# Kernel tuning notes

Hardware: AMD Instinct MI355X
Metric: run time of the kernel (lower is better)

The kernel has to match this reference:

```python
import jax, jax.numpy as jnp
import numpy as np

B, S, D = 4, 128, 4096
H, KV, HD = 32, 8, 128
REP = H // KV  # GQA repeat factor = 4


def setup_inputs() -> dict:
    key = jax.random.key(0)
    ks = jax.random.split(key, 10)
    scale = 0.02
    x = jax.random.normal(ks[0], (B, S, D), dtype=jnp.float32)
    # projection weights stored as (in, out) so y = x @ W + b (== torch Linear)
    wq = jax.random.normal(ks[1], (D, H * HD), dtype=jnp.float32) * scale
    bq = jax.random.normal(ks[2], (H * HD,), dtype=jnp.float32) * scale
    wk = jax.random.normal(ks[3], (D, KV * HD), dtype=jnp.float32) * scale
    bk = jax.random.normal(ks[4], (KV * HD,), dtype=jnp.float32) * scale
    wv = jax.random.normal(ks[5], (D, KV * HD), dtype=jnp.float32) * scale
    bv = jax.random.normal(ks[6], (KV * HD,), dtype=jnp.float32) * scale
    wo = jax.random.normal(ks[7], (H * HD, D), dtype=jnp.float32) * scale
    bo = jax.random.normal(ks[8], (D,), dtype=jnp.float32) * scale
    # rotary frequencies: theta=10000, half-dim = HD//2 = 64
    inv_freq = 1.0 / (10000.0 ** (jnp.arange(0, HD, 2, dtype=jnp.float32) / HD))
    t = jnp.arange(S, dtype=jnp.float32)
    angles = jnp.outer(t, inv_freq)  # (S, 64)
    freqs_cos = jnp.cos(angles)
    freqs_sin = jnp.sin(angles)
    # additive causal mask (S, S): 0 on/below diagonal, -inf above
    mask = jnp.where(jnp.tril(jnp.ones((S, S), dtype=bool)), 0.0, -jnp.inf).astype(jnp.float32)
    cache_k = jnp.zeros((B, S, KV, HD), dtype=jnp.float32)
    cache_v = jnp.zeros((B, S, KV, HD), dtype=jnp.float32)
    return {
        "x": x, "start_pos": 0, "freqs_cos": freqs_cos, "freqs_sin": freqs_sin,
        "mask": mask, "cache_k": cache_k, "cache_v": cache_v,
        "wq": wq, "bq": bq, "wk": wk, "bk": bk, "wv": wv, "bv": bv,
        "wo": wo, "bo": bo,
    }


def _rope(t, cos, sin):
    # t: (B, S, h, HD); treat last dim as HD//2 complex pairs (real, imag)
    tr = t.reshape(*t.shape[:-1], HD // 2, 2)
    tre, tim = tr[..., 0], tr[..., 1]
    c = cos[None, :, None, :]  # (1, S, 1, HD//2)
    s = sin[None, :, None, :]
    out_re = tre * c - tim * s
    out_im = tre * s + tim * c
    return jnp.stack([out_re, out_im], axis=-1).reshape(t.shape)


def reference(x, start_pos, freqs_cos, freqs_sin, mask, cache_k, cache_v,
              wq, bq, wk, bk, wv, bv, wo, bo):
    bsz, seq_len, _ = x.shape
    q = (x @ wq + bq).reshape(bsz, seq_len, H, HD)
    k = (x @ wk + bk).reshape(bsz, seq_len, KV, HD)
    v = (x @ wv + bv).reshape(bsz, seq_len, KV, HD)
    q = _rope(q, freqs_cos, freqs_sin)
    k = _rope(k, freqs_cos, freqs_sin)
    # KV-cache append (functional)
    cache_k = cache_k.at[:bsz, start_pos:start_pos + seq_len].set(k)
    cache_v = cache_v.at[:bsz, start_pos:start_pos + seq_len].set(v)
    keys = cache_k[:bsz, :start_pos + seq_len]    # (B, T, KV, HD)
    vals = cache_v[:bsz, :start_pos + seq_len]
    # GQA head expansion (repeat_interleave on head dim)
    keys = jnp.repeat(keys, REP, axis=2)          # (B, T, H, HD)
    vals = jnp.repeat(vals, REP, axis=2)
    scale = 1.0 / jnp.sqrt(jnp.float32(HD))
    scores = jnp.einsum('bqhd,bkhd->bhqk', q, keys) * scale + mask
    attn = jax.nn.softmax(scores, axis=-1)
    out = jnp.einsum('bhqk,bkhd->bqhd', attn, vals).reshape(bsz, seq_len, H * HD)
    return out @ wo + bo
```

## Files before the change

### kernel.cpp

```cpp
#include <hip/hip_runtime.h>
#include <math.h>


#define B_   4
#define S_   128
#define D_   4096
#define H_   32
#define KV_  8
#define HD_  128
#define M_   (B_ * S_)
#define NQKV 6144
#define SCALE_ 0.088388347648318447f

typedef _Float16 half_t;
typedef half_t f16x8 __attribute__((ext_vector_type(8)));
typedef float  f32x4 __attribute__((ext_vector_type(4)));

__device__ inline void load_lds16(const void* g, void* l) {
    __builtin_amdgcn_global_load_lds((const __attribute__((address_space(1))) void*)g,
                                     (__attribute__((address_space(3))) void*)l,
                                     16, 0, 0);
}

__device__ void transpose_tile(const float* __restrict__ src, int Nsrc, int nsrc0,
                               int ndst0, int k0, int Ntot,
                               half_t* __restrict__ Wt, void* ldsraw) {
    float (*tile)[132] = (float(*)[132])ldsraw;
    const int t = threadIdx.x;
#pragma unroll
    for (int p = 0; p < 8; ++p) {
        int idx = t + p * 256;
        int r = idx >> 5, c4 = idx & 31;
        *(float4*)&tile[r][c4 * 4] =
            *(const float4*)&src[(size_t)(k0 + r) * Nsrc + nsrc0 + c4 * 4];
    }
    __syncthreads();
    const int n = t >> 1, kh = t & 1;
    __align__(16) half_t hs[32];
#pragma unroll
    for (int i = 0; i < 32; ++i)
        hs[i] = (half_t)tile[kh * 32 + i][n];
    size_t ob = ((size_t)(k0 >> 6) * Ntot + ndst0 + n) * 64 + kh * 32;
#pragma unroll
    for (int u = 0; u < 4; ++u)
        *(uint4*)&Wt[ob + u * 8] = *(uint4*)&hs[u * 8];
}

__device__ void gemm_tile(const half_t* __restrict__ A16, const half_t* __restrict__ Wt,
                          float* __restrict__ Part, int N, int m0, int n0,
                          int zi, int kslice, char* lds) {
    half_t (*As)[64] = (half_t(*)[64])lds;
    half_t (*Bs)[64] = (half_t(*)[64])(lds + 16384);
    const int tid = threadIdx.x;
    const int kbase = zi * kslice;
    const int lane = tid & 63;
    const int quad = lane >> 4, l16 = lane & 15;
    const int w = tid >> 6;
    const int wm = (w & 1) * 64, wn = (w >> 1) * 64;
    const int tB = tid & 192;

    f32x4 acc[4][4] = {};

    for (int kc = kbase; kc < kbase + kslice; kc += 64) {
        const half_t* Bslab = Wt + ((size_t)(kc >> 6) * N + n0) * 64;
#pragma unroll
        for (int p = 0; p < 4; ++p) {
            int tb = p * 256 + tB;
            int task = tb + lane;
            int r = task >> 3;
            int os = (task ^ r) & 7;
            load_lds16(&A16[(size_t)(m0 + r) * 4096 + kc + os * 8], (half_t*)As + tb * 8);
            load_lds16(&Bslab[(size_t)r * 64 + os * 8],             (half_t*)Bs + tb * 8);
        }
        __syncthreads();
#pragma unroll
        for (int kk = 0; kk < 2; ++kk) {
            f16x8 af[4], bf[4];
#pragma unroll
            for (int i = 0; i < 4; ++i) {
                int ra = wm + i * 16 + l16;
                int rb = wn + i * 16 + l16;
                int L = kk * 4 + quad;
                af[i] = *(const f16x8*)&As[ra][(L ^ (ra & 7)) * 8];
                bf[i] = *(const f16x8*)&Bs[rb][(L ^ (rb & 7)) * 8];
            }
#pragma unroll
            for (int i = 0; i < 4; ++i)
#pragma unroll
                for (int j = 0; j < 4; ++j)
                    acc[i][j] = __builtin_amdgcn_mfma_f32_16x16x32_f16(af[i], bf[j], acc[i][j], 0, 0, 0);
        }
        __syncthreads();
    }
    float* Cp = Part + (size_t)zi * ((size_t)M_ * N);
#pragma unroll
    for (int i = 0; i < 4; ++i)
#pragma unroll
        for (int j = 0; j < 4; ++j) {
            int col = n0 + wn + j * 16 + l16;
            int rowb = m0 + wm + i * 16 + quad * 4;
#pragma unroll
            for (int rg = 0; rg < 4; ++rg)
                Cp[(size_t)(rowb + rg) * N + col] = acc[i][j][rg];
        }
}

__global__ __launch_bounds__(256)
void prep_qkv(const float* __restrict__ wq, const float* __restrict__ wk,
              const float* __restrict__ wv, const float* __restrict__ x,
              half_t* __restrict__ Wt, half_t* __restrict__ x16) {
    __shared__ __align__(16) char lds[33792];
    const int bx = blockIdx.x;
    if (bx < 3072) {
        int nt = bx % 48, kt = bx / 48;
        const float* src; int Nsrc, ns0, nd0;
        if (nt < 32)      { src = wq; Nsrc = 4096; ns0 = nt * 128;        nd0 = nt * 128; }
        else if (nt < 40) { src = wk; Nsrc = 1024; ns0 = (nt - 32) * 128; nd0 = 4096 + (nt - 32) * 128; }
        else              { src = wv; Nsrc = 1024; ns0 = (nt - 40) * 128; nd0 = 5120 + (nt - 40) * 128; }
        transpose_tile(src, Nsrc, ns0, nd0, kt * 64, NQKV, Wt, lds);
    } else {
        int i0 = (bx - 3072) * 1024 + threadIdx.x;
#pragma unroll
        for (int j = 0; j < 4; ++j) {
            int i = i0 + j * 256;
            float4 f = ((const float4*)x)[i];
            __align__(8) half_t h4[4] = {(half_t)f.x, (half_t)f.y, (half_t)f.z, (half_t)f.w};
            ((uint2*)x16)[i] = *(uint2*)h4;
        }
    }
}

__global__ __launch_bounds__(256, 3)
void gemm_qkv_pack(const half_t* __restrict__ x16, const half_t* __restrict__ Wt,
                   float* __restrict__ Part, int kslice, int gemmBlocks,
                   const float* __restrict__ wo, half_t* __restrict__ WtO) {
    __shared__ __align__(16) char lds[33792];
    const int bx = blockIdx.x;
    if (bx < gemmBlocks) {
        int nb = bx % 48, mb = (bx / 48) & 3, zi = bx / 192;
        gemm_tile(x16, Wt, Part, NQKV, mb * 128, nb * 128, zi, kslice, lds);
    } else {
        int t = bx - gemmBlocks;
        int nt = t & 31, kt = t >> 5;
        transpose_tile(wo, 4096, nt * 128, nt * 128, kt * 64, 4096, WtO, lds);
    }
}

__global__ __launch_bounds__(256)
void wo_trans(const float* __restrict__ wo, half_t* __restrict__ WtO) {
    __shared__ __align__(16) char lds[33792];
    int nt = blockIdx.x & 31, kt = blockIdx.x >> 5;
    transpose_tile(wo, 4096, nt * 128, nt * 128, kt * 64, 4096, WtO, lds);
}

__global__ __launch_bounds__(256, 3)
void gemm_o(const half_t* __restrict__ a16, const half_t* __restrict__ WtO,
            float* __restrict__ Part, int kslice) {
    __shared__ __align__(16) char lds[33792];
    gemm_tile(a16, WtO, Part, 4096, blockIdx.y * 128, blockIdx.x * 128,
              blockIdx.z, kslice, lds);
}

__global__ void qkv_reduce_rope(const float* __restrict__ Part, int nz,
                                const float* __restrict__ bq, const float* __restrict__ bk,
                                const float* __restrict__ bv,
                                const float* __restrict__ fc, const float* __restrict__ fs,
                                half_t* __restrict__ q16, half_t* __restrict__ k16,
                                half_t* __restrict__ vt16) {
    const int row = blockIdx.y;
    const int col = (blockIdx.x * 256 + threadIdx.x) * 2;
    const size_t off = (size_t)row * NQKV + col;
    float2 s = *(const float2*)&Part[off];
    for (int z = 1; z < nz; ++z) {
        float2 p = *(const float2*)&Part[(size_t)z * (M_ * NQKV) + off];
        s.x += p.x; s.y += p.y;
    }
    float2 bi;
    if (col < 4096)      bi = *(const float2*)&bq[col];
    else if (col < 5120) bi = *(const float2*)&bk[col - 4096];
    else                 bi = *(const float2*)&bv[col - 5120];
    s.x += bi.x; s.y += bi.y;
    if (col < 5120) {
        int d2 = (col >> 1) & 63;
        int i = row & 127;
        float c = fc[i * 64 + d2], sn = fs[i * 64 + d2];
        float re = s.x, im = s.y;
        s.x = re * c - im * sn;
        s.y = re * sn + im * c;
    }
    __align__(4) half_t hh[2] = {(half_t)s.x, (half_t)s.y};
    if (col < 4096) {
        *(unsigned int*)&q16[(size_t)row * 4096 + col] = *(unsigned int*)hh;
    } else if (col < 5120) {
        *(unsigned int*)&k16[(size_t)row * 1024 + (col - 4096)] = *(unsigned int*)hh;
    } else {
        int c = col - 5120;
        int kv = c >> 7, d = c & 127;
        int b = row >> 7, i = row & 127;
        size_t base = ((size_t)(b * 8 + kv) * 128 + d) * 128 + i;
        vt16[base]       = hh[0];
        vt16[base + 128] = hh[1];
    }
}

__global__ __launch_bounds__(256, 2)
void fused_attn(const half_t* __restrict__ q16, const half_t* __restrict__ k16,
                const half_t* __restrict__ vt16, half_t* __restrict__ a16) {
    __shared__ __align__(16) half_t Qs[32][136];
    __shared__ __align__(16) half_t Ks[128][136];
    __shared__ float Ps[32][132];
    __shared__ float red[32][16];

    const int tid = threadIdx.x;
    const int qi = blockIdx.x & 3, h = (blockIdx.x >> 2) & 31, b = blockIdx.x >> 7;
    const int kv = h >> 2;
    const int qbase = qi * 32;
    const int lane = tid & 63, w = tid >> 6;
    const int quad = lane >> 4, l16 = lane & 15;
    const int m0 = (w & 1) * 16, half64 = (w >> 1) * 64;

#pragma unroll
    for (int p = 0; p < 2; ++p) {
        int task = tid + p * 256;
        int r = task >> 4, c = task & 15;
        *(uint4*)&Qs[r][c * 8] =
            *(const uint4*)&q16[((size_t)(b * 128 + qbase + r) * 32 + h) * 128 + c * 8];
    }
#pragma unroll
    for (int p = 0; p < 8; ++p) {
        int task = tid + p * 256;
        int r = task >> 4, c = task & 15;
        *(uint4*)&Ks[r][c * 8] =
            *(const uint4*)&k16[((size_t)(b * 128 + r) * 8 + kv) * 128 + c * 8];
    }
    __syncthreads();

    f32x4 s[4] = {};
#pragma unroll
    for (int kc = 0; kc < 4; ++kc) {
        f16x8 af = *(const f16x8*)&Qs[m0 + l16][kc * 32 + quad * 8];
#pragma unroll
        for (int jb = 0; jb < 4; ++jb) {
            f16x8 bf = *(const f16x8*)&Ks[half64 + jb * 16 + l16][kc * 32 + quad * 8];
            s[jb] = __builtin_amdgcn_mfma_f32_16x16x32_f16(af, bf, s[jb], 0, 0, 0);
        }
    }
#pragma unroll
    for (int jb = 0; jb < 4; ++jb) {
        int j = half64 + jb * 16 + l16;
#pragma unroll
        for (int rg = 0; rg < 4; ++rg) {
            int row = m0 + quad * 4 + rg;
            Ps[row][j] = (j <= qbase + row) ? s[jb][rg] * SCALE_ : -1e30f;
        }
    }
    __syncthreads();

    const int r = tid >> 3, seg = tid & 7;
    float mx = -1e30f;
#pragma unroll
    for (int i = 0; i < 16; ++i) mx = fmaxf(mx, Ps[r][seg * 16 + i]);
    red[r][seg] = mx;
    __syncthreads();

    uint4 vstage[8];
#pragma unroll
    for (int p = 0; p < 8; ++p) {
        int task = tid + p * 256;
        int rr = task >> 4, c = task & 15;
        vstage[p] = *(const uint4*)&vt16[((size_t)(b * 8 + kv) * 128 + rr) * 128 + c * 8];
    }
    float m = red[r][0];
#pragma unroll
    for (int i = 1; i < 8; ++i) m = fmaxf(m, red[r][i]);
    float sum = 0.f;
#pragma unroll
    for (int i = 0; i < 16; ++i) {
        float e = __expf(Ps[r][seg * 16 + i] - m);
        Ps[r][seg * 16 + i] = e;
        sum += e;
    }
    red[r][8 + seg] = sum;
#pragma unroll
    for (int p = 0; p < 8; ++p) {
        int task = tid + p * 256;
        int rr = task >> 4, c = task & 15;
        *(uint4*)&Ks[rr][c * 8] = vstage[p];
    }
    __syncthreads();

    float tot = 0.f;
#pragma unroll
    for (int i = 0; i < 8; ++i) tot += red[r][8 + i];
    float inv = 1.0f / tot;
#pragma unroll
    for (int i = 0; i < 16; ++i)
        Qs[r][seg * 16 + i] = (half_t)(Ps[r][seg * 16 + i] * inv);
    __syncthreads();

    f32x4 o[4] = {};
#pragma unroll
    for (int jc = 0; jc < 4; ++jc) {
        f16x8 af = *(const f16x8*)&Qs[m0 + l16][jc * 32 + quad * 8];
#pragma unroll
        for (int db = 0; db < 4; ++db) {
            f16x8 bf = *(const f16x8*)&Ks[half64 + db * 16 + l16][jc * 32 + quad * 8];
            o[db] = __builtin_amdgcn_mfma_f32_16x16x32_f16(af, bf, o[db], 0, 0, 0);
        }
    }
#pragma unroll
    for (int db = 0; db < 4; ++db) {
        int d = half64 + db * 16 + l16;
#pragma unroll
        for (int rg = 0; rg < 4; ++rg) {
            int row = m0 + quad * 4 + rg;
            a16[(size_t)(b * 128 + qbase + row) * 4096 + h * 128 + d] = (half_t)o[db][rg];
        }
    }
}

__global__ void o_reduce(const float* __restrict__ Part, int nz,
                         const float* __restrict__ bo, float* __restrict__ out) {
    const size_t off = (size_t)(blockIdx.x * 256 + threadIdx.x) * 4;
    float4 s = *(const float4*)&Part[off];
    for (int z = 1; z < nz; ++z) {
        float4 p = *(const float4*)&Part[(size_t)z * (M_ * 4096) + off];
        s.x += p.x; s.y += p.y; s.z += p.z; s.w += p.w;
    }
    float4 b = *(const float4*)&bo[off & 4095];
    s.x += b.x; s.y += b.y; s.z += b.z; s.w += b.w;
    *(float4*)&out[off] = s;
}

extern "C" void kernel_launch(void* const* d_in, const int* in_sizes, int n_in,
                              void* d_out, int out_size, void* d_ws, size_t ws_size,
                              hipStream_t stream) {
    const float* x    = (const float*)d_in[0];
    const float* fc   = (const float*)d_in[2];
    const float* fs   = (const float*)d_in[3];
    const float* wq   = (const float*)d_in[7];
    const float* bq   = (const float*)d_in[8];
    const float* wk   = (const float*)d_in[9];
    const float* bk   = (const float*)d_in[10];
    const float* wv   = (const float*)d_in[11];
    const float* bv   = (const float*)d_in[12];
    const float* wo   = (const float*)d_in[13];
    const float* bo   = (const float*)d_in[14];
    float* out = (float*)d_out;

    half_t* x16  = (half_t*)d_ws;
    half_t* a16  = x16 + 2097152;
    half_t* q16  = a16 + 2097152;
    half_t* k16  = q16 + 2097152;
    half_t* vt16 = k16 + 524288;
    half_t* Wt   = vt16 + 524288;

    const size_t fixedB = 65011712;
    const size_t fixedA = fixedB + (size_t)16777216 * 2;
    int z; bool packed;
    if      (ws_size >= fixedA + 4 * (size_t)12582912) { packed = true;  z = 4; }
    else if (ws_size >= fixedA + 2 * (size_t)12582912) { packed = true;  z = 2; }
    else if (ws_size >= fixedB + 4 * (size_t)12582912) { packed = false; z = 4; }
    else                                               { packed = false; z = 2; }
    half_t* WtO  = packed ? Wt + 25165824 : Wt;
    float*  Part = (float*)((char*)d_ws + (packed ? fixedA : fixedB));
    const int kslice = 4096 / z;

    prep_qkv<<<3584, 256, 0, stream>>>(wq, wk, wv, x, Wt, x16);

    gemm_qkv_pack<<<192 * z + (packed ? 2048 : 0), 256, 0, stream>>>(
        x16, Wt, Part, kslice, 192 * z, wo, WtO);

    qkv_reduce_rope<<<dim3(12, 512), 256, 0, stream>>>(Part, z, bq, bk, bv, fc, fs,
                                                       q16, k16, vt16);
    if (!packed)
        wo_trans<<<2048, 256, 0, stream>>>(wo, WtO);

    fused_attn<<<512, 256, 0, stream>>>(q16, k16, vt16, a16);

    gemm_o<<<dim3(32, 4, z), 256, 0, stream>>>(a16, WtO, Part, kslice);
    o_reduce<<<2048, 256, 0, stream>>>(Part, z, bo, out);
}
```

Measured before the change: 295.3 us.

## Fuse split-K reductions, bias and RoPE into GEMM epilogues; overlap Wo transpose with attention

```diff
diff --git a/kernel.cpp b/kernel.cpp
--- a/kernel.cpp
+++ b/kernel.cpp
@@ -44,65 +44,6 @@
 #pragma unroll
     for (int u = 0; u < 4; ++u)
         *(uint4*)&Wt[ob + u * 8] = *(uint4*)&hs[u * 8];
-}
-
-__device__ void gemm_tile(const half_t* __restrict__ A16, const half_t* __restrict__ Wt,
-                          float* __restrict__ Part, int N, int m0, int n0,
-                          int zi, int kslice, char* lds) {
-    half_t (*As)[64] = (half_t(*)[64])lds;
-    half_t (*Bs)[64] = (half_t(*)[64])(lds + 16384);
-    const int tid = threadIdx.x;
-    const int kbase = zi * kslice;
-    const int lane = tid & 63;
-    const int quad = lane >> 4, l16 = lane & 15;
-    const int w = tid >> 6;
-    const int wm = (w & 1) * 64, wn = (w >> 1) * 64;
-    const int tB = tid & 192;
-
-    f32x4 acc[4][4] = {};
-
-    for (int kc = kbase; kc < kbase + kslice; kc += 64) {
-        const half_t* Bslab = Wt + ((size_t)(kc >> 6) * N + n0) * 64;
-#pragma unroll
-        for (int p = 0; p < 4; ++p) {
-            int tb = p * 256 + tB;
-            int task = tb + lane;
-            int r = task >> 3;
-            int os = (task ^ r) & 7;
-            load_lds16(&A16[(size_t)(m0 + r) * 4096 + kc + os * 8], (half_t*)As + tb * 8);
-            load_lds16(&Bslab[(size_t)r * 64 + os * 8],             (half_t*)Bs + tb * 8);
-        }
-        __syncthreads();
-#pragma unroll
-        for (int kk = 0; kk < 2; ++kk) {
-            f16x8 af[4], bf[4];
-#pragma unroll
-            for (int i = 0; i < 4; ++i) {
-                int ra = wm + i * 16 + l16;
-                int rb = wn + i * 16 + l16;
-                int L = kk * 4 + quad;
-                af[i] = *(const f16x8*)&As[ra][(L ^ (ra & 7)) * 8];
-                bf[i] = *(const f16x8*)&Bs[rb][(L ^ (rb & 7)) * 8];
-            }
-#pragma unroll
-            for (int i = 0; i < 4; ++i)
-#pragma unroll
-                for (int j = 0; j < 4; ++j)
-                    acc[i][j] = __builtin_amdgcn_mfma_f32_16x16x32_f16(af[i], bf[j], acc[i][j], 0, 0, 0);
-        }
-        __syncthreads();
-    }
-    float* Cp = Part + (size_t)zi * ((size_t)M_ * N);
-#pragma unroll
-    for (int i = 0; i < 4; ++i)
-#pragma unroll
-        for (int j = 0; j < 4; ++j) {
-            int col = n0 + wn + j * 16 + l16;
-            int rowb = m0 + wm + i * 16 + quad * 4;
-#pragma unroll
-            for (int rg = 0; rg < 4; ++rg)
-                Cp[(size_t)(rowb + rg) * N + col] = acc[i][j][rg];
-        }
 }
 
 __global__ __launch_bounds__(256)
@@ -130,86 +71,156 @@
     }
 }
 
-__global__ __launch_bounds__(256, 3)
-void gemm_qkv_pack(const half_t* __restrict__ x16, const half_t* __restrict__ Wt,
-                   float* __restrict__ Part, int kslice, int gemmBlocks,
-                   const float* __restrict__ wo, half_t* __restrict__ WtO) {
-    __shared__ __align__(16) char lds[33792];
-    const int bx = blockIdx.x;
-    if (bx < gemmBlocks) {
-        int nb = bx % 48, mb = (bx / 48) & 3, zi = bx / 192;
-        gemm_tile(x16, Wt, Part, NQKV, mb * 128, nb * 128, zi, kslice, lds);
+__global__ __launch_bounds__(512)
+void gemm_qkv_fused(const half_t* __restrict__ x16, const half_t* __restrict__ Wt,
+                    const float* __restrict__ bq, const float* __restrict__ bk,
+                    const float* __restrict__ bv, const float* __restrict__ fc,
+                    const float* __restrict__ fs, half_t* __restrict__ q16,
+                    half_t* __restrict__ k16, half_t* __restrict__ vt16) {
+    __shared__ __align__(16) char lds[67584];
+    const int tid = threadIdx.x;
+    const int nb = blockIdx.x % 48, mb = blockIdx.x / 48;
+    const int m0 = mb * 128, n0 = nb * 128;
+    const int g = tid >> 8;
+    const int lane = tid & 63;
+    const int quad = lane >> 4, l16 = lane & 15;
+    const int w4 = (tid >> 6) & 3;
+    const int wm = (w4 & 1) * 64, wn = (w4 >> 1) * 64;
+    const int tB = tid & 192;
+
+    half_t (*As)[64] = (half_t(*)[64])(lds + g * 32768);
+    half_t (*Bs)[64] = (half_t(*)[64])(lds + g * 32768 + 16384);
+
+    f32x4 acc[4][4] = {};
+    const int kend = g * 2048 + 2048;
+    for (int kc = g * 2048; kc < kend; kc += 64) {
+        const half_t* Bslab = Wt + ((size_t)(kc >> 6) * NQKV + n0) * 64;
+#pragma unroll
+        for (int p = 0; p < 4; ++p) {
+            int tb = p * 256 + tB;
+            int task = tb + lane;
+            int r = task >> 3;
+            int os = (task ^ r) & 7;
+            load_lds16(&x16[(size_t)(m0 + r) * 4096 + kc + os * 8], (half_t*)As + tb * 8);
+            load_lds16(&Bslab[(size_t)r * 64 + os * 8],             (half_t*)Bs + tb * 8);
+        }
+        __syncthreads();
+#pragma unroll
+        for (int kk = 0; kk < 2; ++kk) {
+            f16x8 af[4], bf[4];
+#pragma unroll
+            for (int i = 0; i < 4; ++i) {
+                int ra = wm + i * 16 + l16;
+                int rb = wn + i * 16 + l16;
+                int L = kk * 4 + quad;
+                af[i] = *(const f16x8*)&As[ra][(L ^ (ra & 7)) * 8];
+                bf[i] = *(const f16x8*)&Bs[rb][(L ^ (rb & 7)) * 8];
+            }
+#pragma unroll
+            for (int i = 0; i < 4; ++i)
+#pragma unroll
+                for (int j = 0; j < 4; ++j)
+                    acc[i][j] = __builtin_amdgcn_mfma_f32_16x16x32_f16(af[i], bf[j], acc[i][j], 0, 0, 0);
+        }
+        __syncthreads();
+    }
+
+    float (*Tf)[132] = (float(*)[132])lds;
+    if (g == 1) {
+#pragma unroll
+        for (int i = 0; i < 4; ++i)
+#pragma unroll
+            for (int j = 0; j < 4; ++j)
+#pragma unroll
+                for (int rg = 0; rg < 4; ++rg)
+                    Tf[wm + i * 16 + quad * 4 + rg][wn + j * 16 + l16] = acc[i][j][rg];
+    }
+    __syncthreads();
+    if (g == 0) {
+#pragma unroll
+        for (int i = 0; i < 4; ++i)
+#pragma unroll
+            for (int j = 0; j < 4; ++j)
+#pragma unroll
+                for (int rg = 0; rg < 4; ++rg)
+                    acc[i][j][rg] += Tf[wm + i * 16 + quad * 4 + rg][wn + j * 16 + l16];
+    }
+
+    if (n0 < 5120) {
+        if (g == 0) {
+            const bool isQ = n0 < 4096;
+            const float* bias = isQ ? bq : bk;
+            const int bOff = isQ ? 0 : 4096;
+            half_t* dst = isQ ? q16 : k16;
+            const int ldd = isQ ? 4096 : 1024;
+#pragma unroll
+            for (int i = 0; i < 4; ++i)
+#pragma unroll
+                for (int j = 0; j < 4; ++j) {
+                    const int col = n0 + wn + j * 16 + l16;
+                    const int d2 = (col >> 1) & 63;
+                    const float bcol = bias[col - bOff];
+#pragma unroll
+                    for (int rg = 0; rg < 4; ++rg) {
+                        const int row = m0 + wm + i * 16 + quad * 4 + rg;
+                        float v = acc[i][j][rg] + bcol;
+                        float o = __shfl_xor(v, 1);
+                        const int iloc = row & 127;
+                        const float c = fc[iloc * 64 + d2], sn = fs[iloc * 64 + d2];
+                        float ov = (l16 & 1) ? (o * sn + v * c)
+                                             : (v * c - o * sn);
+                        float o2 = __shfl_xor(ov, 1);
+                        if (!(l16 & 1)) {
+                            __align__(4) half_t hh[2] = {(half_t)ov, (half_t)o2};
+                            *(unsigned int*)&dst[(size_t)row * ldd + (col - bOff)] =
+                                *(unsigned int*)hh;
+                        }
+                    }
+                }
+        }
     } else {
-        int t = bx - gemmBlocks;
-        int nt = t & 31, kt = t >> 5;
-        transpose_tile(wo, 4096, nt * 128, nt * 128, kt * 64, 4096, WtO, lds);
-    }
-}
-
-__global__ __launch_bounds__(256)
-void wo_trans(const float* __restrict__ wo, half_t* __restrict__ WtO) {
-    __shared__ __align__(16) char lds[33792];
-    int nt = blockIdx.x & 31, kt = blockIdx.x >> 5;
-    transpose_tile(wo, 4096, nt * 128, nt * 128, kt * 64, 4096, WtO, lds);
-}
-
-__global__ __launch_bounds__(256, 3)
-void gemm_o(const half_t* __restrict__ a16, const half_t* __restrict__ WtO,
-            float* __restrict__ Part, int kslice) {
-    __shared__ __align__(16) char lds[33792];
-    gemm_tile(a16, WtO, Part, 4096, blockIdx.y * 128, blockIdx.x * 128,
-              blockIdx.z, kslice, lds);
-}
-
-__global__ void qkv_reduce_rope(const float* __restrict__ Part, int nz,
-                                const float* __restrict__ bq, const float* __restrict__ bk,
-                                const float* __restrict__ bv,
-                                const float* __restrict__ fc, const float* __restrict__ fs,
-                                half_t* __restrict__ q16, half_t* __restrict__ k16,
-                                half_t* __restrict__ vt16) {
-    const int row = blockIdx.y;
-    const int col = (blockIdx.x * 256 + threadIdx.x) * 2;
-    const size_t off = (size_t)row * NQKV + col;
-    float2 s = *(const float2*)&Part[off];
-    for (int z = 1; z < nz; ++z) {
-        float2 p = *(const float2*)&Part[(size_t)z * (M_ * NQKV) + off];
-        s.x += p.x; s.y += p.y;
-    }
-    float2 bi;
-    if (col < 4096)      bi = *(const float2*)&bq[col];
-    else if (col < 5120) bi = *(const float2*)&bk[col - 4096];
-    else                 bi = *(const float2*)&bv[col - 5120];
-    s.x += bi.x; s.y += bi.y;
-    if (col < 5120) {
-        int d2 = (col >> 1) & 63;
-        int i = row & 127;
-        float c = fc[i * 64 + d2], sn = fs[i * 64 + d2];
-        float re = s.x, im = s.y;
-        s.x = re * c - im * sn;
-        s.y = re * sn + im * c;
-    }
-    __align__(4) half_t hh[2] = {(half_t)s.x, (half_t)s.y};
-    if (col < 4096) {
-        *(unsigned int*)&q16[(size_t)row * 4096 + col] = *(unsigned int*)hh;
-    } else if (col < 5120) {
-        *(unsigned int*)&k16[(size_t)row * 1024 + (col - 4096)] = *(unsigned int*)hh;
-    } else {
-        int c = col - 5120;
-        int kv = c >> 7, d = c & 127;
-        int b = row >> 7, i = row & 127;
-        size_t base = ((size_t)(b * 8 + kv) * 128 + d) * 128 + i;
-        vt16[base]       = hh[0];
-        vt16[base + 128] = hh[1];
+        __syncthreads();
+        half_t (*Th)[136] = (half_t(*)[136])lds;
+        if (g == 0) {
+#pragma unroll
+            for (int i = 0; i < 4; ++i)
+#pragma unroll
+                for (int j = 0; j < 4; ++j) {
+                    const int cl = wn + j * 16 + l16;
+                    const float bcol = bv[n0 - 5120 + cl];
+#pragma unroll
+                    for (int rg = 0; rg < 4; ++rg)
+                        Th[wm + i * 16 + quad * 4 + rg][cl] = (half_t)(acc[i][j][rg] + bcol);
+                }
+        }
+        __syncthreads();
+        const int d = tid >> 2, iq = tid & 3;
+        const int kv = (n0 - 5120) >> 7;
+        __align__(16) half_t hs[32];
+#pragma unroll
+        for (int u = 0; u < 32; ++u) hs[u] = Th[iq * 32 + u][d];
+        size_t base = ((size_t)(mb * 8 + kv) * 128 + d) * 128 + iq * 32;
+#pragma unroll
+        for (int u = 0; u < 4; ++u)
+            *(uint4*)&vt16[base + u * 8] = *(uint4*)&hs[u * 8];
     }
 }
 
 __global__ __launch_bounds__(256, 2)
-void fused_attn(const half_t* __restrict__ q16, const half_t* __restrict__ k16,
-                const half_t* __restrict__ vt16, half_t* __restrict__ a16) {
-    __shared__ __align__(16) half_t Qs[32][136];
-    __shared__ __align__(16) half_t Ks[128][136];
-    __shared__ float Ps[32][132];
-    __shared__ float red[32][16];
+void attn_wo(const half_t* __restrict__ q16, const half_t* __restrict__ k16,
+             const half_t* __restrict__ vt16, half_t* __restrict__ a16,
+             const float* __restrict__ wo, half_t* __restrict__ WtO) {
+    __shared__ __align__(16) char lds[62464];
+    if (blockIdx.x >= 512) {
+        int t = blockIdx.x - 512;
+        transpose_tile(wo, 4096, (t & 31) * 128, (t & 31) * 128, (t >> 5) * 64,
+                       4096, WtO, lds);
+        return;
+    }
+    half_t (*Qs)[136] = (half_t(*)[136])lds;
+    half_t (*Ks)[136] = (half_t(*)[136])(lds + 8704);
+    float (*Ps)[132]  = (float(*)[132])(lds + 43520);
+    float (*red)[16]  = (float(*)[16])(lds + 60416);
 
     const int tid = threadIdx.x;
     const int qi = blockIdx.x & 3, h = (blockIdx.x >> 2) & 31, b = blockIdx.x >> 7;
@@ -319,17 +330,86 @@
     }
 }
 
-__global__ void o_reduce(const float* __restrict__ Part, int nz,
-                         const float* __restrict__ bo, float* __restrict__ out) {
-    const size_t off = (size_t)(blockIdx.x * 256 + threadIdx.x) * 4;
-    float4 s = *(const float4*)&Part[off];
-    for (int z = 1; z < nz; ++z) {
-        float4 p = *(const float4*)&Part[(size_t)z * (M_ * 4096) + off];
-        s.x += p.x; s.y += p.y; s.z += p.z; s.w += p.w;
-    }
-    float4 b = *(const float4*)&bo[off & 4095];
-    s.x += b.x; s.y += b.y; s.z += b.z; s.w += b.w;
-    *(float4*)&out[off] = s;
+__global__ __launch_bounds__(512)
+void gemm_o_fused(const half_t* __restrict__ a16, const half_t* __restrict__ WtO,
+                  const float* __restrict__ bo, float* __restrict__ out) {
+    __shared__ __align__(16) char lds[49152];
+    const int tid = threadIdx.x;
+    const int nb = blockIdx.x & 31, mb = blockIdx.x >> 5;
+    const int m0 = mb * 64, n0 = nb * 128;
+    const int g = tid >> 8;
+    const int lane = tid & 63;
+    const int quad = lane >> 4, l16 = lane & 15;
+    const int w4 = (tid >> 6) & 3;
+    const int wn = w4 * 32;
+    const int tB = tid & 192;
+
+    half_t (*As)[64] = (half_t(*)[64])(lds + g * 24576);
+    half_t (*Bs)[64] = (half_t(*)[64])(lds + g * 24576 + 8192);
+
+    f32x4 acc[4][2] = {};
+    const int kend = g * 2048 + 2048;
+    for (int kc = g * 2048; kc < kend; kc += 64) {
+        const half_t* Bslab = WtO + ((size_t)(kc >> 6) * 4096 + n0) * 64;
+#pragma unroll
+        for (int p = 0; p < 4; ++p) {
+            int tb = p * 256 + tB;
+            int task = tb + lane;
+            int r = task >> 3;
+            int os = (task ^ r) & 7;
+            load_lds16(&Bslab[(size_t)r * 64 + os * 8], (half_t*)Bs + tb * 8);
+            if (p < 2)
+                load_lds16(&a16[(size_t)(m0 + r) * 4096 + kc + os * 8], (half_t*)As + tb * 8);
+        }
+        __syncthreads();
+#pragma unroll
+        for (int kk = 0; kk < 2; ++kk) {
+            f16x8 af[4], bf[2];
+#pragma unroll
+            for (int i = 0; i < 4; ++i) {
+                int ra = i * 16 + l16;
+                af[i] = *(const f16x8*)&As[ra][((kk * 4 + quad) ^ (ra & 7)) * 8];
+            }
+#pragma unroll
+            for (int j = 0; j < 2; ++j) {
+                int rb = wn + j * 16 + l16;
+                bf[j] = *(const f16x8*)&Bs[rb][((kk * 4 + quad) ^ (rb & 7)) * 8];
+            }
+#pragma unroll
+            for (int i = 0; i < 4; ++i)
+#pragma unroll
+                for (int j = 0; j < 2; ++j)
+                    acc[i][j] = __builtin_amdgcn_mfma_f32_16x16x32_f16(af[i], bf[j], acc[i][j], 0, 0, 0);
+        }
+        __syncthreads();
+    }
+
+    float (*Tf)[132] = (float(*)[132])lds;
+    if (g == 1) {
+#pragma unroll
+        for (int i = 0; i < 4; ++i)
+#pragma unroll
+            for (int j = 0; j < 2; ++j)
+#pragma unroll
+                for (int rg = 0; rg < 4; ++rg)
+                    Tf[i * 16 + quad * 4 + rg][wn + j * 16 + l16] = acc[i][j][rg];
+    }
+    __syncthreads();
+    if (g == 0) {
+#pragma unroll
+        for (int i = 0; i < 4; ++i)
+#pragma unroll
+            for (int j = 0; j < 2; ++j) {
+                const int col = n0 + wn + j * 16 + l16;
+                const float bcol = bo[col];
+#pragma unroll
+                for (int rg = 0; rg < 4; ++rg) {
+                    const int row = m0 + i * 16 + quad * 4 + rg;
+                    out[(size_t)row * 4096 + col] =
+                        acc[i][j][rg] + Tf[i * 16 + quad * 4 + rg][wn + j * 16 + l16] + bcol;
+                }
+            }
+    }
 }
 
 extern "C" void kernel_launch(void* const* d_in, const int* in_sizes, int n_in,
@@ -354,30 +434,14 @@
     half_t* k16  = q16 + 2097152;
     half_t* vt16 = k16 + 524288;
     half_t* Wt   = vt16 + 524288;
-
-    const size_t fixedB = 65011712;
-    const size_t fixedA = fixedB + (size_t)16777216 * 2;
-    int z; bool packed;
-    if      (ws_size >= fixedA + 4 * (size_t)12582912) { packed = true;  z = 4; }
-    else if (ws_size >= fixedA + 2 * (size_t)12582912) { packed = true;  z = 2; }
-    else if (ws_size >= fixedB + 4 * (size_t)12582912) { packed = false; z = 4; }
-    else                                               { packed = false; z = 2; }
-    half_t* WtO  = packed ? Wt + 25165824 : Wt;
-    float*  Part = (float*)((char*)d_ws + (packed ? fixedA : fixedB));
-    const int kslice = 4096 / z;
+    half_t* WtO  = Wt;
 
     prep_qkv<<<3584, 256, 0, stream>>>(wq, wk, wv, x, Wt, x16);
 
-    gemm_qkv_pack<<<192 * z + (packed ? 2048 : 0), 256, 0, stream>>>(
-        x16, Wt, Part, kslice, 192 * z, wo, WtO);
-
-    qkv_reduce_rope<<<dim3(12, 512), 256, 0, stream>>>(Part, z, bq, bk, bv, fc, fs,
-                                                       q16, k16, vt16);
-    if (!packed)
-        wo_trans<<<2048, 256, 0, stream>>>(wo, WtO);
-
-    fused_attn<<<512, 256, 0, stream>>>(q16, k16, vt16, a16);
-
-    gemm_o<<<dim3(32, 4, z), 256, 0, stream>>>(a16, WtO, Part, kslice);
-    o_reduce<<<2048, 256, 0, stream>>>(Part, z, bo, out);
-}
+    gemm_qkv_fused<<<192, 512, 0, stream>>>(x16, Wt, bq, bk, bv, fc, fs,
+                                            q16, k16, vt16);
+
+    attn_wo<<<2560, 256, 0, stream>>>(q16, k16, vt16, a16, wo, WtO);
+
+    gemm_o_fused<<<256, 512, 0, stream>>>(a16, WtO, bo, out);
+}
```

Result: slower. 314.5 us (+6.5%).

## Triple-buffer GEMM K-loop with BK=32 stages and swizzle transpose LDS tile

Applied to the files above, without the earlier changes.

```diff
diff --git a/kernel.cpp b/kernel.cpp
--- a/kernel.cpp
+++ b/kernel.cpp
@@ -31,78 +31,24 @@
     for (int p = 0; p < 8; ++p) {
         int idx = t + p * 256;
         int r = idx >> 5, c4 = idx & 31;
-        *(float4*)&tile[r][c4 * 4] =
+        *(float4*)&tile[r][((c4 ^ ((r >> 3) & 7)) * 4)] =
             *(const float4*)&src[(size_t)(k0 + r) * Nsrc + nsrc0 + c4 * 4];
     }
     __syncthreads();
-    const int n = t >> 1, kh = t & 1;
-    __align__(16) half_t hs[32];
-#pragma unroll
-    for (int i = 0; i < 32; ++i)
-        hs[i] = (half_t)tile[kh * 32 + i][n];
-    size_t ob = ((size_t)(k0 >> 6) * Ntot + ndst0 + n) * 64 + kh * 32;
-#pragma unroll
-    for (int u = 0; u < 4; ++u)
-        *(uint4*)&Wt[ob + u * 8] = *(uint4*)&hs[u * 8];
-}
-
-__device__ void gemm_tile(const half_t* __restrict__ A16, const half_t* __restrict__ Wt,
-                          float* __restrict__ Part, int N, int m0, int n0,
-                          int zi, int kslice, char* lds) {
-    half_t (*As)[64] = (half_t(*)[64])lds;
-    half_t (*Bs)[64] = (half_t(*)[64])(lds + 16384);
-    const int tid = threadIdx.x;
-    const int kbase = zi * kslice;
-    const int lane = tid & 63;
-    const int quad = lane >> 4, l16 = lane & 15;
-    const int w = tid >> 6;
-    const int wm = (w & 1) * 64, wn = (w >> 1) * 64;
-    const int tB = tid & 192;
-
-    f32x4 acc[4][4] = {};
-
-    for (int kc = kbase; kc < kbase + kslice; kc += 64) {
-        const half_t* Bslab = Wt + ((size_t)(kc >> 6) * N + n0) * 64;
-#pragma unroll
-        for (int p = 0; p < 4; ++p) {
-            int tb = p * 256 + tB;
-            int task = tb + lane;
-            int r = task >> 3;
-            int os = (task ^ r) & 7;
-            load_lds16(&A16[(size_t)(m0 + r) * 4096 + kc + os * 8], (half_t*)As + tb * 8);
-            load_lds16(&Bslab[(size_t)r * 64 + os * 8],             (half_t*)Bs + tb * 8);
-        }
-        __syncthreads();
-#pragma unroll
-        for (int kk = 0; kk < 2; ++kk) {
-            f16x8 af[4], bf[4];
-#pragma unroll
-            for (int i = 0; i < 4; ++i) {
-                int ra = wm + i * 16 + l16;
-                int rb = wn + i * 16 + l16;
-                int L = kk * 4 + quad;
-                af[i] = *(const f16x8*)&As[ra][(L ^ (ra & 7)) * 8];
-                bf[i] = *(const f16x8*)&Bs[rb][(L ^ (rb & 7)) * 8];
-            }
-#pragma unroll
-            for (int i = 0; i < 4; ++i)
-#pragma unroll
-                for (int j = 0; j < 4; ++j)
-                    acc[i][j] = __builtin_amdgcn_mfma_f32_16x16x32_f16(af[i], bf[j], acc[i][j], 0, 0, 0);
-        }
-        __syncthreads();
-    }
-    float* Cp = Part + (size_t)zi * ((size_t)M_ * N);
-#pragma unroll
-    for (int i = 0; i < 4; ++i)
-#pragma unroll
-        for (int j = 0; j < 4; ++j) {
-            int col = n0 + wn + j * 16 + l16;
-            int rowb = m0 + wm + i * 16 + quad * 4;
-#pragma unroll
-            for (int rg = 0; rg < 4; ++rg)
-                Cp[(size_t)(rowb + rg) * N + col] = acc[i][j][rg];
-        }
+    const int kh = (t >> 2) & 1, cc = t & 3, dd = t >> 3;
+    const int rbase = kh * 32 + cc * 8;
+    const int h3 = 4 * kh + cc;
+    size_t tb = ((size_t)(k0 >> 6) * Ntot + ndst0) * 64;
+#pragma unroll
+    for (int u = 0; u < 4; ++u) {
+        int n = u * 32 + dd;
+        int pc = ((n >> 2) ^ h3) * 4 + (n & 3);
+        __align__(16) half_t hs[8];
+#pragma unroll
+        for (int i = 0; i < 8; ++i)
+            hs[i] = (half_t)tile[rbase + i][pc];
+        *(uint4*)&Wt[tb + (size_t)u * 2048 + t * 8] = *(uint4*)hs;
+    }
 }
 
 __global__ __launch_bounds__(256)
@@ -130,35 +76,113 @@
     }
 }
 
+__device__ __forceinline__ void stage_bk32(const half_t* __restrict__ A,
+                                           const half_t* __restrict__ Bbase,
+                                           int N, int m0, int n0, int kc,
+                                           half_t* AsD, half_t* BsD, int tid) {
+    const int lane = tid & 63, tB = tid & 192;
+    const half_t* Bslab = Bbase + ((size_t)(kc >> 6) * N + n0) * 64 + ((kc >> 5) & 1) * 32;
+#pragma unroll
+    for (int p = 0; p < 2; ++p) {
+        int tb = p * 256 + tB;
+        int task = tb + lane;
+        int r = task >> 2, c = task & 3;
+        load_lds16(&A[(size_t)(m0 + r) * 4096 + kc + c * 8], AsD + tb * 8);
+        load_lds16(&Bslab[(size_t)r * 64 + c * 8],           BsD + tb * 8);
+    }
+}
+
+__device__ __forceinline__ void compute_bk32(const half_t* AsD, const half_t* BsD,
+                                             int tid, f32x4 (&acc)[4][4]) {
+    const int lane = tid & 63;
+    const int quad = lane >> 4, l16 = lane & 15;
+    const int w = tid >> 6;
+    const int wm = (w & 1) * 64, wn = (w >> 1) * 64;
+    half_t (*As)[32] = (half_t(*)[32])AsD;
+    half_t (*Bs)[32] = (half_t(*)[32])BsD;
+    f16x8 af[4], bf[4];
+#pragma unroll
+    for (int i = 0; i < 4; ++i)
+        af[i] = *(const f16x8*)&As[wm + i * 16 + l16][quad * 8];
+#pragma unroll
+    for (int j = 0; j < 4; ++j)
+        bf[j] = *(const f16x8*)&Bs[wn + j * 16 + l16][quad * 8];
+#pragma unroll
+    for (int i = 0; i < 4; ++i)
+#pragma unroll
+        for (int j = 0; j < 4; ++j)
+            acc[i][j] = __builtin_amdgcn_mfma_f32_16x16x32_f16(af[i], bf[j], acc[i][j], 0, 0, 0);
+}
+
+__device__ __forceinline__ void fence4() {
+    asm volatile("s_waitcnt vmcnt(4)" ::: "memory");
+    __builtin_amdgcn_s_barrier();
+    __builtin_amdgcn_sched_barrier(0);
+}
+__device__ __forceinline__ void fence0() {
+    asm volatile("s_waitcnt vmcnt(0)" ::: "memory");
+    __builtin_amdgcn_s_barrier();
+    __builtin_amdgcn_sched_barrier(0);
+}
+
+__device__ __forceinline__ void gemm128_bk32(const half_t* __restrict__ A,
+                                             const half_t* __restrict__ Bbase,
+                                             int N, int m0, int n0, int kbase,
+                                             int ksteps, char* lds,
+                                             f32x4 (&acc)[4][4]) {
+    const int tid = threadIdx.x;
+    half_t* As0 = (half_t*)lds;
+    half_t* Bs0 = (half_t*)(lds + 24576);
+    stage_bk32(A, Bbase, N, m0, n0, kbase,      As0,        Bs0,        tid);
+    stage_bk32(A, Bbase, N, m0, n0, kbase + 32, As0 + 4096, Bs0 + 4096, tid);
+    fence4();
+    int cur = 0, pf = 2;
+    for (int it = 0; it < ksteps - 2; ++it) {
+        stage_bk32(A, Bbase, N, m0, n0, kbase + (it + 2) * 32,
+                   As0 + pf * 4096, Bs0 + pf * 4096, tid);
+        compute_bk32(As0 + cur * 4096, Bs0 + cur * 4096, tid, acc);
+        fence4();
+        cur = (cur == 2) ? 0 : cur + 1;
+        pf  = (pf  == 2) ? 0 : pf  + 1;
+    }
+    compute_bk32(As0 + cur * 4096, Bs0 + cur * 4096, tid, acc);
+    fence0();
+    cur = (cur == 2) ? 0 : cur + 1;
+    compute_bk32(As0 + cur * 4096, Bs0 + cur * 4096, tid, acc);
+}
+
 __global__ __launch_bounds__(256, 3)
 void gemm_qkv_pack(const half_t* __restrict__ x16, const half_t* __restrict__ Wt,
                    float* __restrict__ Part, int kslice, int gemmBlocks,
                    const float* __restrict__ wo, half_t* __restrict__ WtO) {
-    __shared__ __align__(16) char lds[33792];
+    __shared__ __align__(16) char lds[49152];
     const int bx = blockIdx.x;
     if (bx < gemmBlocks) {
-        int nb = bx % 48, mb = (bx / 48) & 3, zi = bx / 192;
-        gemm_tile(x16, Wt, Part, NQKV, mb * 128, nb * 128, zi, kslice, lds);
+        const int nb = bx % 48, mb = (bx / 48) & 3, zi = bx / 192;
+        const int m0 = mb * 128, n0 = nb * 128;
+        f32x4 acc[4][4] = {};
+        gemm128_bk32(x16, Wt, NQKV, m0, n0, zi * kslice, kslice / 32, lds, acc);
+        const int tid = threadIdx.x;
+        const int lane = tid & 63;
+        const int quad = lane >> 4, l16 = lane & 15;
+        const int w = tid >> 6;
+        const int wm = (w & 1) * 64, wn = (w >> 1) * 64;
+        float* Cp = Part + (size_t)zi * ((size_t)M_ * NQKV);
+#pragma unroll
+        for (int i = 0; i < 4; ++i)
+#pragma unroll
+            for (int j = 0; j < 4; ++j) {
+                int col = n0 + wn + j * 16 + l16;
+                int rowb = m0 + wm + i * 16 + quad * 4;
+#pragma unroll
+                for (int rg = 0; rg < 4; ++rg)
+                    Cp[(size_t)(rowb + rg) * NQKV + col] = acc[i][j][rg];
+            }
     } else {
         int t = bx - gemmBlocks;
-        int nt = t & 31, kt = t >> 5;
-        transpose_tile(wo, 4096, nt * 128, nt * 128, kt * 64, 4096, WtO, lds);
-    }
-}
-
-__global__ __launch_bounds__(256)
-void wo_trans(const float* __restrict__ wo, half_t* __restrict__ WtO) {
-    __shared__ __align__(16) char lds[33792];
-    int nt = blockIdx.x & 31, kt = blockIdx.x >> 5;
-    transpose_tile(wo, 4096, nt * 128, nt * 128, kt * 64, 4096, WtO, lds);
-}
-
-__global__ __launch_bounds__(256, 3)
-void gemm_o(const half_t* __restrict__ a16, const half_t* __restrict__ WtO,
-            float* __restrict__ Part, int kslice) {
-    __shared__ __align__(16) char lds[33792];
-    gemm_tile(a16, WtO, Part, 4096, blockIdx.y * 128, blockIdx.x * 128,
-              blockIdx.z, kslice, lds);
+        transpose_tile(wo, 4096, (t & 31) * 128, (t & 31) * 128, (t >> 5) * 64,
+                       4096, WtO, lds);
+    }
 }
 
 __global__ void qkv_reduce_rope(const float* __restrict__ Part, int nz,
@@ -172,7 +196,7 @@
     const size_t off = (size_t)row * NQKV + col;
     float2 s = *(const float2*)&Part[off];
     for (int z = 1; z < nz; ++z) {
-        float2 p = *(const float2*)&Part[(size_t)z * (M_ * NQKV) + off];
+        float2 p = *(const float2*)&Part[(size_t)z * ((size_t)M_ * NQKV) + off];
         s.x += p.x; s.y += p.y;
     }
     float2 bi;
@@ -206,10 +230,11 @@
 __global__ __launch_bounds__(256, 2)
 void fused_attn(const half_t* __restrict__ q16, const half_t* __restrict__ k16,
                 const half_t* __restrict__ vt16, half_t* __restrict__ a16) {
-    __shared__ __align__(16) half_t Qs[32][136];
-    __shared__ __align__(16) half_t Ks[128][136];
-    __shared__ float Ps[32][132];
-    __shared__ float red[32][16];
+    __shared__ __align__(16) char lds[62464];
+    half_t (*Qs)[136] = (half_t(*)[136])lds;
+    half_t (*Ks)[136] = (half_t(*)[136])(lds + 8704);
+    float (*Ps)[132]  = (float(*)[132])(lds + 43520);
+    float (*red)[16]  = (float(*)[16])(lds + 60416);
 
     const int tid = threadIdx.x;
     const int qi = blockIdx.x & 3, h = (blockIdx.x >> 2) & 31, b = blockIdx.x >> 7;
@@ -319,12 +344,39 @@
     }
 }
 
+__global__ __launch_bounds__(256, 3)
+void gemm_o(const half_t* __restrict__ a16, const half_t* __restrict__ WtO,
+            float* __restrict__ Part, int kslice) {
+    __shared__ __align__(16) char lds[49152];
+    const int bx = blockIdx.x;
+    const int nb = bx % 32, mb = (bx / 32) & 3, zi = bx / 128;
+    const int m0 = mb * 128, n0 = nb * 128;
+    f32x4 acc[4][4] = {};
+    gemm128_bk32(a16, WtO, 4096, m0, n0, zi * kslice, kslice / 32, lds, acc);
+    const int tid = threadIdx.x;
+    const int lane = tid & 63;
+    const int quad = lane >> 4, l16 = lane & 15;
+    const int w = tid >> 6;
+    const int wm = (w & 1) * 64, wn = (w >> 1) * 64;
+    float* Cp = Part + (size_t)zi * ((size_t)M_ * 4096);
+#pragma unroll
+    for (int i = 0; i < 4; ++i)
+#pragma unroll
+        for (int j = 0; j < 4; ++j) {
+            int col = n0 + wn + j * 16 + l16;
+            int rowb = m0 + wm + i * 16 + quad * 4;
+#pragma unroll
+            for (int rg = 0; rg < 4; ++rg)
+                Cp[(size_t)(rowb + rg) * 4096 + col] = acc[i][j][rg];
+        }
+}
+
 __global__ void o_reduce(const float* __restrict__ Part, int nz,
                          const float* __restrict__ bo, float* __restrict__ out) {
     const size_t off = (size_t)(blockIdx.x * 256 + threadIdx.x) * 4;
     float4 s = *(const float4*)&Part[off];
     for (int z = 1; z < nz; ++z) {
-        float4 p = *(const float4*)&Part[(size_t)z * (M_ * 4096) + off];
+        float4 p = *(const float4*)&Part[(size_t)z * ((size_t)M_ * 4096) + off];
         s.x += p.x; s.y += p.y; s.z += p.z; s.w += p.w;
     }
     float4 b = *(const float4*)&bo[off & 4095];
@@ -354,30 +406,23 @@
     half_t* k16  = q16 + 2097152;
     half_t* vt16 = k16 + 524288;
     half_t* Wt   = vt16 + 524288;
-
-    const size_t fixedB = 65011712;
-    const size_t fixedA = fixedB + (size_t)16777216 * 2;
-    int z; bool packed;
-    if      (ws_size >= fixedA + 4 * (size_t)12582912) { packed = true;  z = 4; }
-    else if (ws_size >= fixedA + 2 * (size_t)12582912) { packed = true;  z = 2; }
-    else if (ws_size >= fixedB + 4 * (size_t)12582912) { packed = false; z = 4; }
-    else                                               { packed = false; z = 2; }
-    half_t* WtO  = packed ? Wt + 25165824 : Wt;
-    float*  Part = (float*)((char*)d_ws + (packed ? fixedA : fixedB));
+    half_t* WtO  = Wt + 25165824;
+    const size_t fixedA = 65011712 + (size_t)16777216 * 2;
+    float* Part = (float*)((char*)d_ws + fixedA);
+
+    int z = (ws_size >= fixedA + 4 * (size_t)12582912) ? 4 : 2;
     const int kslice = 4096 / z;
 
     prep_qkv<<<3584, 256, 0, stream>>>(wq, wk, wv, x, Wt, x16);
 
-    gemm_qkv_pack<<<192 * z + (packed ? 2048 : 0), 256, 0, stream>>>(
-        x16, Wt, Part, kslice, 192 * z, wo, WtO);
-
-    qkv_reduce_rope<<<dim3(12, 512), 256, 0, stream>>>(Part, z, bq, bk, bv, fc, fs,
-                                                       q16, k16, vt16);
-    if (!packed)
-        wo_trans<<<2048, 256, 0, stream>>>(wo, WtO);
+    gemm_qkv_pack<<<192 * z + 2048, 256, 0, stream>>>(x16, Wt, Part, kslice,
+                                                      192 * z, wo, WtO);
+
+    qkv_reduce_rope<<<dim3(12, 512), 256, 0, stream>>>(Part, z, bq, bk, bv,
+                                                       fc, fs, q16, k16, vt16);
 
     fused_attn<<<512, 256, 0, stream>>>(q16, k16, vt16, a16);
 
-    gemm_o<<<dim3(32, 4, z), 256, 0, stream>>>(a16, WtO, Part, kslice);
+    gemm_o<<<128 * z, 256, 0, stream>>>(a16, WtO, Part, kslice);
     o_reduce<<<2048, 256, 0, stream>>>(Part, z, bo, out);
 }
```

Measured after the change: 295.2 us. No clear change (-0.0%).
